# Performance work log

Measured on AMD Instinct MI355X. Metric: run time of the kernel, lower is better.

## Reference

```python
import jax, jax.numpy as jnp
import numpy as np

N = 4096      # nodes
IN = 512      # input_size
D = 128       # output_size per head
H = 4         # num_heads
SLOPE = 0.2   # leaky relu negative slope
NEG = -1e30   # masked-out logit value (finite to keep softmax grad-safe)


def setup_inputs() -> dict:
    key = jax.random.key(0)
    ks = jax.random.split(key, 8)
    stdv = 1.0 / np.sqrt(H * D)
    inputs = jax.random.normal(ks[0], (N, IN), jnp.float32)
    adjacency = jax.random.randint(ks[1], (N, N), 0, 2).astype(jnp.float32)  # dense 0/1 mask
    weight = jax.random.uniform(ks[2], (IN, H * D), jnp.float32, -stdv, stdv)
    weight_u = jax.random.uniform(ks[3], (H, D, 1), jnp.float32, -1.0, 1.0)
    weight_v = jax.random.uniform(ks[4], (H, D, 1), jnp.float32, -1.0, 1.0)
    bias = jax.random.uniform(ks[5], (1, H * D), jnp.float32, -stdv, stdv)
    proj_w = jax.random.normal(ks[6], (IN, H * D), jnp.float32) * 0.02
    proj_b = jnp.zeros((H * D,), jnp.float32)
    return {"inputs": inputs, "adjacency": adjacency, "weight": weight,
            "weight_u": weight_u, "weight_v": weight_v, "bias": bias,
            "proj_w": proj_w, "proj_b": proj_b}


def reference(inputs, adjacency, weight, weight_u, weight_v, bias, proj_w, proj_b):
    # support: [H, N, D]
    support = (inputs @ weight).reshape(N, H, D).transpose(1, 0, 2)
    # f1: per-source scores [H, 1, N]; f2: per-dest scores [H, N, 1]
    f1 = jnp.einsum('hnd,hdo->hn', support, weight_u)[:, None, :]
    f2 = jnp.einsum('hnd,hdo->hn', support, weight_v)[:, :, None]
    logits = f1 + f2                                  # [H, N, N]
    w = jnp.where(logits >= 0, logits, SLOPE * logits)  # leaky_relu
    masked = w * adjacency[None]                      # [H, N, N]
    # torch to_sparse keeps nonzero entries; sparse softmax treats the rest as -inf
    mask = masked != 0
    z = jnp.where(mask, masked, NEG)
    attn = jax.nn.softmax(z, axis=-1) * mask          # rows with no edges -> all zeros
    out = jnp.einsum('hij,hjd->hid', attn, support)   # [H, N, D]
    out = out.transpose(1, 0, 2).reshape(N, H * D)
    out = out + bias
    out = out + inputs @ proj_w + proj_b              # residual projection
    return out
```

## Files before the change

### kernel.cpp

```cpp
#include <hip/hip_runtime.h>

#define NN 4096
#define IND 512
#define HD 512
#define NH 4
#define DH 128
#define K3 1536

typedef __attribute__((ext_vector_type(8))) short bf16x8;
typedef __attribute__((ext_vector_type(4))) float f32x4;
typedef __attribute__((ext_vector_type(4))) unsigned short us4;
typedef __attribute__((ext_vector_type(8))) unsigned short us8;

typedef __attribute__((address_space(3))) void lds_void;
typedef const __attribute__((address_space(1))) void glob_void;

__device__ __forceinline__ void gll16(const void* g, void* l) {
  __builtin_amdgcn_global_load_lds((glob_void*)g, (lds_void*)l, 16, 0, 0);
}

__device__ __forceinline__ unsigned short f2bf(float x) {
  union { float f; unsigned u; } a; a.f = x;
  unsigned r = a.u + 0x7FFFu + ((a.u >> 16) & 1u);
  return (unsigned short)(r >> 16);
}
__device__ __forceinline__ float bf2f(unsigned short b) {
  union { float f; unsigned u; } a; a.u = ((unsigned)b) << 16;
  return a.f;
}

__global__ __launch_bounds__(256) void prep_inputs(const float* __restrict__ x,
                                                   unsigned short* __restrict__ A3) {
  int idx = blockIdx.x * 256 + threadIdx.x;
  int n = idx >> 9, c = idx & 511;
  float v = x[idx];
  unsigned short hi = f2bf(v);
  unsigned short lo = f2bf(v - bf2f(hi));
  size_t base = (size_t)n * K3;
  A3[base + c] = hi;
  A3[base + 512 + c] = hi;
  A3[base + 1024 + c] = lo;
}

__global__ __launch_bounds__(256) void prep_weights(const float* __restrict__ w,
                                                    const float* __restrict__ pw,
                                                    unsigned short* __restrict__ B3T,
                                                    unsigned short* __restrict__ PhT) {
  int idx = blockIdx.x * 256 + threadIdx.x;
  int c = idx >> 9, k = idx & 511;
  float v = w[(size_t)k * HD + c];
  unsigned short hi = f2bf(v);
  unsigned short lo = f2bf(v - bf2f(hi));
  size_t base = (size_t)c * K3;
  B3T[base + k] = hi;
  B3T[base + 512 + k] = lo;
  B3T[base + 1024 + k] = hi;
  float p = pw[(size_t)k * HD + c];
  PhT[(size_t)c * IND + k] = f2bf(p);
}

__global__ __launch_bounds__(256) void gemm_kernel(
    const unsigned short* __restrict__ A3, const unsigned short* __restrict__ B3T,
    const unsigned short* __restrict__ PhT,
    float* __restrict__ support, unsigned short* __restrict__ ST,
    float* __restrict__ resid,
    const float* __restrict__ projb, const float* __restrict__ bias) {
  const int z = blockIdx.z;
  const unsigned short* Bp = z ? PhT : B3T;
  const int ldb = z ? IND : K3;
  const int K = z ? IND : K3;
  const int m0 = blockIdx.x * 128;
  const int n0 = blockIdx.y * 64;
  const int tid = threadIdx.x;
  const int lane = tid & 63;
  const int wv = tid >> 6;
  const int wm = wv & 1, wn = wv >> 1;

  __shared__ unsigned short As[2][128 * 64];
  __shared__ unsigned short Bs[2][64 * 64];

  f32x4 acc[4][2];
#pragma unroll
  for (int a = 0; a < 4; ++a)
#pragma unroll
    for (int b = 0; b < 2; ++b) acc[a][b] = (f32x4){0.f, 0.f, 0.f, 0.f};

  auto STAGE = [&](int buf, int k0) {
#pragma unroll
    for (int s = 0; s < 4; ++s) {
      int c = s * 256 + tid;
      int rr = c >> 3, sl = c & 7;
      int ko = sl ^ (rr & 7);
      gll16(A3 + (size_t)(m0 + rr) * K3 + k0 + ko * 8, &As[buf][c * 8]);
    }
#pragma unroll
    for (int s = 0; s < 2; ++s) {
      int c = s * 256 + tid;
      int rr = c >> 3, sl = c & 7;
      int ko = sl ^ (rr & 7);
      gll16(Bp + (size_t)(n0 + rr) * ldb + k0 + ko * 8, &Bs[buf][c * 8]);
    }
  };

  STAGE(0, 0);
  __syncthreads();

  const int lrow = lane & 15;
  const int kgc = lane >> 4;
  const int sx = lrow & 7;
  int buf = 0;
  for (int k0 = 0; k0 < K; k0 += 64) {
    if (k0 + 64 < K) STAGE(buf ^ 1, k0 + 64);
#pragma unroll
    for (int js = 0; js < 64; js += 32) {
      int cb = (js >> 3) + kgc;
      bf16x8 af[4], bfr[2];
#pragma unroll
      for (int mf = 0; mf < 4; ++mf) {
        int row = wm * 64 + mf * 16 + lrow;
        af[mf] = *(const bf16x8*)(&As[buf][row * 64 + (cb ^ sx) * 8]);
      }
#pragma unroll
      for (int nf = 0; nf < 2; ++nf) {
        int row = wn * 32 + nf * 16 + lrow;
        bfr[nf] = *(const bf16x8*)(&Bs[buf][row * 64 + (cb ^ sx) * 8]);
      }
#pragma unroll
      for (int mf = 0; mf < 4; ++mf)
#pragma unroll
        for (int nf = 0; nf < 2; ++nf)
          acc[mf][nf] = __builtin_amdgcn_mfma_f32_16x16x32_bf16(af[mf], bfr[nf], acc[mf][nf], 0, 0, 0);
    }
    __syncthreads();
    buf ^= 1;
  }

  const int lrow4 = (lane >> 4) * 4;
  const int lcol = lane & 15;
  if (z == 0) {
#pragma unroll
    for (int mf = 0; mf < 4; ++mf) {
#pragma unroll
      for (int nf = 0; nf < 2; ++nf) {
        int rg = m0 + wm * 64 + mf * 16 + lrow4;
        int cg = n0 + wn * 32 + nf * 16 + lcol;
#pragma unroll
        for (int q = 0; q < 4; ++q)
          support[(size_t)(rg + q) * HD + cg] = acc[mf][nf][q];
        us4 st4;
#pragma unroll
        for (int q = 0; q < 4; ++q) st4[q] = f2bf(acc[mf][nf][q]);
        *(us4*)(ST + (size_t)cg * NN + rg) = st4;
      }
    }
  } else {
#pragma unroll
    for (int mf = 0; mf < 4; ++mf) {
#pragma unroll
      for (int nf = 0; nf < 2; ++nf) {
        int rg = m0 + wm * 64 + mf * 16 + lrow4;
        int cg = n0 + wn * 32 + nf * 16 + lcol;
        float addv = projb[cg] + bias[cg];
#pragma unroll
        for (int q = 0; q < 4; ++q)
          resid[(size_t)(rg + q) * HD + cg] = acc[mf][nf][q] + addv;
      }
    }
  }
}

__global__ __launch_bounds__(256) void f1f2_kernel(const float* __restrict__ support,
                                                   const float* __restrict__ wu,
                                                   const float* __restrict__ wv,
                                                   float* __restrict__ g1,
                                                   float* __restrict__ g2) {
  int lane = threadIdx.x & 63;
  int n = blockIdx.x * 4 + (threadIdx.x >> 6);
  const float* srow = support + (size_t)n * HD + lane * 8;
  int h = lane >> 4;
  int d0 = (lane * 8) & 127;
  const float* u = wu + h * DH + d0;
  const float* v = wv + h * DH + d0;
  float du = 0.f, dv = 0.f;
#pragma unroll
  for (int e = 0; e < 8; ++e) {
    float s = srow[e];
    du += s * u[e];
    dv += s * v[e];
  }
#pragma unroll
  for (int off = 1; off < 16; off <<= 1) {
    du += __shfl_xor(du, off);
    dv += __shfl_xor(dv, off);
  }
  if ((lane & 15) == 0) {
    const float L2E = 1.4426950408889634f;
    g1[h * NN + n] = du * L2E;
    g2[h * NN + n] = dv * L2E;
  }
}

__global__ __launch_bounds__(256) void ballot_kernel(const float* __restrict__ adj,
                                                     unsigned long long* __restrict__ bm) {
  int i = blockIdx.x;
  int tid = threadIdx.x, lane = tid & 63, wv = tid >> 6;
  const float* arow = adj + (size_t)i * NN;
#pragma unroll 4
  for (int it = 0; it < 16; ++it) {
    int j = it * 256 + tid;
    unsigned long long b = __ballot(arow[j] != 0.0f);
    if (lane == 0) bm[(size_t)i * 64 + it * 4 + wv] = b;
  }
}

__global__ __launch_bounds__(256) void attn_kernel(
    const unsigned short* __restrict__ ST,
    const unsigned long long* __restrict__ bm,
    const float* __restrict__ g1, const float* __restrict__ g2,
    float* __restrict__ P, float* __restrict__ S) {
  const int bx = blockIdx.x;
  const int by = blockIdx.y;
  const int bz = blockIdx.z;
  const int tid = threadIdx.x;
  const int lane = tid & 63;
  const int w = tid >> 6;

  __shared__ unsigned short tile[2][128 * 64];
  __shared__ unsigned long long bml[32 * 64];
  __shared__ float g1l[2048];

  {
    const unsigned long long* bsrc = bm + (size_t)bx * 64 * 64 + bz * 32;
#pragma unroll
    for (int s = 0; s < 8; ++s) {
      int idx = s * 256 + tid;
      int wd = idx & 31, r = idx >> 5;
      bml[wd * 64 + r] = bsrc[(size_t)r * 64 + wd];
    }
    const float* gsrc = g1 + by * NN + bz * 2048;
#pragma unroll
    for (int s = 0; s < 2; ++s) {
      int idx = s * 256 + tid;
      *(f32x4*)(g1l + idx * 4) = *(const f32x4*)(gsrc + idx * 4);
    }
  }

  const int il = lane & 15;
  const int kg = lane >> 4;
  const int r = w * 16 + il;
  const int ig = bx * 64 + r;
  const float g2v = g2[by * NN + ig];
  const float g2v5 = 0.2f * g2v;
  const unsigned short* stbase = ST + (size_t)by * 128 * NN + bz * 2048;

  auto STAGE = [&](int buf, int jt) {
#pragma unroll
    for (int s = 0; s < 4; ++s) {
      int c = s * 256 + tid;
      int rr = c >> 3, sl = c & 7;
      int jq = sl ^ (rr & 7);
      gll16(stbase + (size_t)rr * NN + jt + jq * 8, &tile[buf][c * 8]);
    }
  };

  STAGE(0, 0);
  __syncthreads();

  bf16x8 ones;
#pragma unroll
  for (int e = 0; e < 8; ++e) ones[e] = (short)0x3F80;

  f32x4 acc[8];
#pragma unroll
  for (int d = 0; d < 8; ++d) acc[d] = (f32x4){0.f, 0.f, 0.f, 0.f};
  f32x4 asum = (f32x4){0.f, 0.f, 0.f, 0.f};

  const char* bmlB = (const char*)bml;
  const int sx = il & 7;
  int buf = 0;

  for (int jt = 0; jt < 2048; jt += 64) {
    if (jt + 64 < 2048) STAGE(buf ^ 1, jt + 64);
#pragma unroll
    for (int js = 0; js < 64; js += 32) {
      int cb = (js >> 3) + kg;
      bf16x8 bc[8];
#pragma unroll
      for (int d = 0; d < 8; ++d)
        bc[d] = *(const bf16x8*)(&tile[buf][(il + d * 16) * 64 + (cb ^ sx) * 8]);

      int jw = jt + js;
      int b = (jw >> 3) + kg;
      unsigned mby = (unsigned char)bmlB[((b >> 3) * 64 + r) * 8 + (b & 7)];
      union F8 { f32x4 v[2]; float f[8]; } gc;
      gc.v[0] = *(const f32x4*)(g1l + jw + kg * 8);
      gc.v[1] = *(const f32x4*)(g1l + jw + kg * 8 + 4);
      float p[8];
#pragma unroll
      for (int e = 0; e < 8; ++e) {
        float a = gc.f[e] + g2v;
        float bb = __builtin_fmaf(0.2f, gc.f[e], g2v5);
        float m = fmaxf(a, bb);
        float pe = __builtin_amdgcn_exp2f(m);
        int sext = -(int)((mby >> e) & 1u);
        union { float f; unsigned u; } pu; pu.f = pe;
        pu.u &= (unsigned)sext;
        p[e] = pu.f;
      }
      union { unsigned u[4]; bf16x8 v; } af;
#pragma unroll
      for (int e2 = 0; e2 < 4; ++e2) {
        unsigned pk;
        asm("v_cvt_pk_bf16_f32 %0, %1, %2" : "=v"(pk) : "v"(p[2 * e2]), "v"(p[2 * e2 + 1]));
        af.u[e2] = pk;
      }
#pragma unroll
      for (int d = 0; d < 8; ++d)
        acc[d] = __builtin_amdgcn_mfma_f32_16x16x32_bf16(af.v, bc[d], acc[d], 0, 0, 0);
      asum = __builtin_amdgcn_mfma_f32_16x16x32_bf16(af.v, ones, asum, 0, 0, 0);
    }
    __syncthreads();
    buf ^= 1;
  }

  float* Pp = P + (size_t)bz * NN * HD;
#pragma unroll
  for (int d = 0; d < 8; ++d) {
    int cg = by * 128 + d * 16 + il;
#pragma unroll
    for (int q = 0; q < 4; ++q) {
      int rg = bx * 64 + w * 16 + kg * 4 + q;
      Pp[(size_t)rg * HD + cg] = acc[d][q];
    }
  }
  if (il == 0) {
#pragma unroll
    for (int q = 0; q < 4; ++q) {
      int rg = bx * 64 + w * 16 + kg * 4 + q;
      S[((size_t)bz * 4 + by) * NN + rg] = asum[q];
    }
  }
}

__global__ __launch_bounds__(256) void merge_kernel(const float* __restrict__ P,
                                                    const float* __restrict__ S,
                                                    const float* __restrict__ resid,
                                                    float* __restrict__ out) {
  int idx = blockIdx.x * 256 + threadIdx.x;
  int i = idx >> 7;
  int c = (idx & 127) * 4;
  int h = c >> 7;
  f32x4 v0 = *(const f32x4*)(P + (size_t)i * HD + c);
  f32x4 v1 = *(const f32x4*)(P + (size_t)(NN + i) * HD + c);
  float s = S[(size_t)h * NN + i] + S[(size_t)(4 + h) * NN + i];
  float rs = s > 0.0f ? 1.0f / s : 0.0f;
  f32x4 rr = *(const f32x4*)(resid + (size_t)i * HD + c);
  f32x4 o;
#pragma unroll
  for (int q = 0; q < 4; ++q) o[q] = (v0[q] + v1[q]) * rs + rr[q];
  *(f32x4*)(out + (size_t)i * HD + c) = o;
}

extern "C" void kernel_launch(void* const* d_in, const int* in_sizes, int n_in,
                              void* d_out, int out_size, void* d_ws, size_t ws_size,
                              hipStream_t stream) {
  const float* inputs = (const float*)d_in[0];
  const float* adj = (const float*)d_in[1];
  const float* weight = (const float*)d_in[2];
  const float* wu = (const float*)d_in[3];
  const float* wv = (const float*)d_in[4];
  const float* bias = (const float*)d_in[5];
  const float* projw = (const float*)d_in[6];
  const float* projb = (const float*)d_in[7];
  float* out = (float*)d_out;

  char* ws = (char*)d_ws;
  size_t off = 0;
  unsigned short* A3 = (unsigned short*)(ws + off); off += (size_t)NN * K3 * 2;
  unsigned short* B3T = (unsigned short*)(ws + off); off += (size_t)HD * K3 * 2;
  unsigned short* PhT = (unsigned short*)(ws + off); off += (size_t)HD * IND * 2;
  float* support = (float*)(ws + off); off += (size_t)NN * HD * 4;
  unsigned short* ST = (unsigned short*)(ws + off); off += (size_t)HD * NN * 2;
  float* resid = (float*)(ws + off); off += (size_t)NN * HD * 4;
  float* g1 = (float*)(ws + off); off += (size_t)NH * NN * 4;
  float* g2 = (float*)(ws + off); off += (size_t)NH * NN * 4;
  unsigned long long* bm = (unsigned long long*)(ws + off); off += (size_t)NN * 64 * 8;

  float* P = (float*)(ws + 0);
  float* S = (float*)(ws + (size_t)17 * 1024 * 1024);

  prep_inputs<<<(NN * IND) / 256, 256, 0, stream>>>(inputs, A3);
  prep_weights<<<(IND * HD) / 256, 256, 0, stream>>>(weight, projw, B3T, PhT);
  gemm_kernel<<<dim3(32, 8, 2), 256, 0, stream>>>(A3, B3T, PhT, support, ST, resid, projb, bias);
  f1f2_kernel<<<NN / 4, 256, 0, stream>>>(support, wu, wv, g1, g2);
  ballot_kernel<<<NN, 256, 0, stream>>>(adj, bm);
  attn_kernel<<<dim3(64, 4, 2), 256, 0, stream>>>(ST, bm, g1, g2, P, S);
  merge_kernel<<<2048, 256, 0, stream>>>(P, S, resid, out);
}
```

Before: 208.6 us.

## Fuse f1/f2 into GEMM epilogue, merge attention split-K in-block, drop merge kernel

The GEMM now uses 128x128 tiles with an XCD-aware block remap. It computes the per-head f1/f2 scores in its epilogue and writes ST through an LDS transpose for coalesced stores, which removes the support buffer and the f1f2 kernel. The attention kernel now splits the key dimension across four waves inside one block, each with its own double-buffered tile and no block-level barriers. It reduces the partial sums through LDS and writes the normalized output plus residual directly, which removes the P/S buffers and the merge kernel. The ballot mask is stored transposed so the attention loop can read it with strided byte loads, with prefetch managed by explicit vmcnt waits. The risks are fewer GEMM blocks and higher register pressure, plus correctness depending on the hand-counted vmcnt.

Result: faster. 200.0 us (-4.1%).

```diff
diff --git a/kernel.cpp b/kernel.cpp
--- a/kernel.cpp
+++ b/kernel.cpp
@@ -62,303 +62,334 @@
 __global__ __launch_bounds__(256) void gemm_kernel(
     const unsigned short* __restrict__ A3, const unsigned short* __restrict__ B3T,
     const unsigned short* __restrict__ PhT,
-    float* __restrict__ support, unsigned short* __restrict__ ST,
-    float* __restrict__ resid,
+    unsigned short* __restrict__ ST, float* __restrict__ resid,
+    float* __restrict__ g1, float* __restrict__ g2,
+    const float* __restrict__ wu, const float* __restrict__ wv,
     const float* __restrict__ projb, const float* __restrict__ bias) {
   const int z = blockIdx.z;
+  int L = blockIdx.x + 32 * blockIdx.y;
+  int xcd = L & 7, idx = L >> 3;
+  const int by = idx & 3;
+  const int bx = (idx >> 2) * 8 + xcd;
   const unsigned short* Bp = z ? PhT : B3T;
   const int ldb = z ? IND : K3;
   const int K = z ? IND : K3;
-  const int m0 = blockIdx.x * 128;
-  const int n0 = blockIdx.y * 64;
+  const int m0 = bx * 128;
+  const int n0 = by * 128;
   const int tid = threadIdx.x;
   const int lane = tid & 63;
-  const int wv = tid >> 6;
-  const int wm = wv & 1, wn = wv >> 1;
-
-  __shared__ unsigned short As[2][128 * 64];
-  __shared__ unsigned short Bs[2][64 * 64];
-
-  f32x4 acc[4][2];
+  const int wvv_ = tid >> 6;
+  const int wm = wvv_ & 1, wn = wvv_ >> 1;
+  const int lrow = lane & 15;
+  const int kg = lane >> 4;
+
+  __shared__ __align__(16) unsigned short sh[32768];
+
+  f32x4 acc[4][4];
 #pragma unroll
   for (int a = 0; a < 4; ++a)
 #pragma unroll
-    for (int b = 0; b < 2; ++b) acc[a][b] = (f32x4){0.f, 0.f, 0.f, 0.f};
+    for (int b = 0; b < 4; ++b) acc[a][b] = (f32x4){0.f, 0.f, 0.f, 0.f};
 
   auto STAGE = [&](int buf, int k0) {
+    unsigned short* Asb = sh + buf * 8192;
+    unsigned short* Bsb = sh + 16384 + buf * 8192;
 #pragma unroll
     for (int s = 0; s < 4; ++s) {
       int c = s * 256 + tid;
       int rr = c >> 3, sl = c & 7;
       int ko = sl ^ (rr & 7);
-      gll16(A3 + (size_t)(m0 + rr) * K3 + k0 + ko * 8, &As[buf][c * 8]);
-    }
-#pragma unroll
-    for (int s = 0; s < 2; ++s) {
+      gll16(A3 + (size_t)(m0 + rr) * K3 + k0 + ko * 8, Asb + c * 8);
+    }
+#pragma unroll
+    for (int s = 0; s < 4; ++s) {
       int c = s * 256 + tid;
       int rr = c >> 3, sl = c & 7;
       int ko = sl ^ (rr & 7);
-      gll16(Bp + (size_t)(n0 + rr) * ldb + k0 + ko * 8, &Bs[buf][c * 8]);
+      gll16(Bp + (size_t)(n0 + rr) * ldb + k0 + ko * 8, Bsb + c * 8);
     }
   };
 
   STAGE(0, 0);
   __syncthreads();
 
-  const int lrow = lane & 15;
-  const int kgc = lane >> 4;
-  const int sx = lrow & 7;
   int buf = 0;
   for (int k0 = 0; k0 < K; k0 += 64) {
     if (k0 + 64 < K) STAGE(buf ^ 1, k0 + 64);
-#pragma unroll
-    for (int js = 0; js < 64; js += 32) {
-      int cb = (js >> 3) + kgc;
-      bf16x8 af[4], bfr[2];
+    const unsigned short* Asb = sh + buf * 8192;
+    const unsigned short* Bsb = sh + 16384 + buf * 8192;
+#pragma unroll
+    for (int ks = 0; ks < 2; ++ks) {
+      int cb = ks * 4 + kg;
+      bf16x8 af[4], bfr[4];
 #pragma unroll
       for (int mf = 0; mf < 4; ++mf) {
         int row = wm * 64 + mf * 16 + lrow;
-        af[mf] = *(const bf16x8*)(&As[buf][row * 64 + (cb ^ sx) * 8]);
+        af[mf] = *(const bf16x8*)(Asb + row * 64 + (cb ^ (row & 7)) * 8);
       }
 #pragma unroll
-      for (int nf = 0; nf < 2; ++nf) {
-        int row = wn * 32 + nf * 16 + lrow;
-        bfr[nf] = *(const bf16x8*)(&Bs[buf][row * 64 + (cb ^ sx) * 8]);
+      for (int nf = 0; nf < 4; ++nf) {
+        int row = wn * 64 + nf * 16 + lrow;
+        bfr[nf] = *(const bf16x8*)(Bsb + row * 64 + (cb ^ (row & 7)) * 8);
       }
 #pragma unroll
       for (int mf = 0; mf < 4; ++mf)
 #pragma unroll
-        for (int nf = 0; nf < 2; ++nf)
+        for (int nf = 0; nf < 4; ++nf)
           acc[mf][nf] = __builtin_amdgcn_mfma_f32_16x16x32_bf16(af[mf], bfr[nf], acc[mf][nf], 0, 0, 0);
     }
     __syncthreads();
     buf ^= 1;
   }
 
-  const int lrow4 = (lane >> 4) * 4;
   const int lcol = lane & 15;
   if (z == 0) {
-#pragma unroll
-    for (int mf = 0; mf < 4; ++mf) {
-#pragma unroll
-      for (int nf = 0; nf < 2; ++nf) {
-        int rg = m0 + wm * 64 + mf * 16 + lrow4;
-        int cg = n0 + wn * 32 + nf * 16 + lcol;
-#pragma unroll
-        for (int q = 0; q < 4; ++q)
-          support[(size_t)(rg + q) * HD + cg] = acc[mf][nf][q];
+    float wuv[4], wvvv[4];
+#pragma unroll
+    for (int nf = 0; nf < 4; ++nf) {
+      int cg = n0 + wn * 64 + nf * 16 + lcol;
+      wuv[nf] = wu[cg]; wvvv[nf] = wv[cg];
+    }
+    float du[4][4], dv[4][4];
+#pragma unroll
+    for (int mf = 0; mf < 4; ++mf)
+#pragma unroll
+      for (int q = 0; q < 4; ++q) {
+        float a = 0.f, b = 0.f;
+#pragma unroll
+        for (int nf = 0; nf < 4; ++nf) {
+          a += acc[mf][nf][q] * wuv[nf];
+          b += acc[mf][nf][q] * wvvv[nf];
+        }
+#pragma unroll
+        for (int m = 1; m < 16; m <<= 1) {
+          a += __shfl_xor(a, m);
+          b += __shfl_xor(b, m);
+        }
+        du[mf][q] = a; dv[mf][q] = b;
+      }
+    float* f12 = (float*)(sh + 17920);
+    if (lcol == 0) {
+#pragma unroll
+      for (int mf = 0; mf < 4; ++mf)
+#pragma unroll
+        for (int q = 0; q < 4; ++q) {
+          int rowl = wm * 64 + mf * 16 + kg * 4 + q;
+          f12[wn * 128 + rowl] = du[mf][q];
+          f12[256 + wn * 128 + rowl] = dv[mf][q];
+        }
+    }
+    unsigned short* lst = sh;
+#pragma unroll
+    for (int mf = 0; mf < 4; ++mf)
+#pragma unroll
+      for (int nf = 0; nf < 4; ++nf) {
+        int coll = wn * 64 + nf * 16 + lcol;
+        int row4 = wm * 64 + mf * 16 + kg * 4;
         us4 st4;
 #pragma unroll
         for (int q = 0; q < 4; ++q) st4[q] = f2bf(acc[mf][nf][q]);
-        *(us4*)(ST + (size_t)cg * NN + rg) = st4;
+        *(us4*)(&lst[coll * 136 + row4]) = st4;
       }
+    __syncthreads();
+    {
+      int row = tid & 127, sel = tid >> 7;
+      float vs = f12[sel * 256 + row] + f12[sel * 256 + 128 + row];
+      float* gp = sel ? g2 : g1;
+      gp[by * NN + m0 + row] = vs * 1.4426950408889634f;
+    }
+#pragma unroll
+    for (int k = 0; k < 8; ++k) {
+      int col = k * 16 + (tid >> 4);
+      int chunk = tid & 15;
+      us8 v = *(const us8*)(&lst[col * 136 + chunk * 8]);
+      *(us8*)(ST + (size_t)(n0 + col) * NN + m0 + chunk * 8) = v;
     }
   } else {
 #pragma unroll
-    for (int mf = 0; mf < 4; ++mf) {
-#pragma unroll
-      for (int nf = 0; nf < 2; ++nf) {
-        int rg = m0 + wm * 64 + mf * 16 + lrow4;
-        int cg = n0 + wn * 32 + nf * 16 + lcol;
+    for (int mf = 0; mf < 4; ++mf)
+#pragma unroll
+      for (int nf = 0; nf < 4; ++nf) {
+        int rg = m0 + wm * 64 + mf * 16 + kg * 4;
+        int cg = n0 + wn * 64 + nf * 16 + lcol;
         float addv = projb[cg] + bias[cg];
 #pragma unroll
         for (int q = 0; q < 4; ++q)
           resid[(size_t)(rg + q) * HD + cg] = acc[mf][nf][q] + addv;
       }
-    }
-  }
-}
-
-__global__ __launch_bounds__(256) void f1f2_kernel(const float* __restrict__ support,
-                                                   const float* __restrict__ wu,
-                                                   const float* __restrict__ wv,
-                                                   float* __restrict__ g1,
-                                                   float* __restrict__ g2) {
-  int lane = threadIdx.x & 63;
-  int n = blockIdx.x * 4 + (threadIdx.x >> 6);
-  const float* srow = support + (size_t)n * HD + lane * 8;
-  int h = lane >> 4;
-  int d0 = (lane * 8) & 127;
-  const float* u = wu + h * DH + d0;
-  const float* v = wv + h * DH + d0;
-  float du = 0.f, dv = 0.f;
-#pragma unroll
-  for (int e = 0; e < 8; ++e) {
-    float s = srow[e];
-    du += s * u[e];
-    dv += s * v[e];
-  }
-#pragma unroll
-  for (int off = 1; off < 16; off <<= 1) {
-    du += __shfl_xor(du, off);
-    dv += __shfl_xor(dv, off);
-  }
-  if ((lane & 15) == 0) {
-    const float L2E = 1.4426950408889634f;
-    g1[h * NN + n] = du * L2E;
-    g2[h * NN + n] = dv * L2E;
   }
 }
 
 __global__ __launch_bounds__(256) void ballot_kernel(const float* __restrict__ adj,
-                                                     unsigned long long* __restrict__ bm) {
+                                                     unsigned long long* __restrict__ bmT) {
   int i = blockIdx.x;
-  int tid = threadIdx.x, lane = tid & 63, wv = tid >> 6;
+  int tid = threadIdx.x, lane = tid & 63, wvv_ = tid >> 6;
   const float* arow = adj + (size_t)i * NN;
 #pragma unroll 4
   for (int it = 0; it < 16; ++it) {
     int j = it * 256 + tid;
     unsigned long long b = __ballot(arow[j] != 0.0f);
-    if (lane == 0) bm[(size_t)i * 64 + it * 4 + wv] = b;
+    if (lane == 0) bmT[(size_t)(it * 4 + wvv_) * NN + i] = b;
   }
 }
 
 __global__ __launch_bounds__(256) void attn_kernel(
     const unsigned short* __restrict__ ST,
-    const unsigned long long* __restrict__ bm,
+    const unsigned long long* __restrict__ bmT,
     const float* __restrict__ g1, const float* __restrict__ g2,
-    float* __restrict__ P, float* __restrict__ S) {
+    const float* __restrict__ resid, float* __restrict__ out) {
   const int bx = blockIdx.x;
   const int by = blockIdx.y;
-  const int bz = blockIdx.z;
   const int tid = threadIdx.x;
   const int lane = tid & 63;
   const int w = tid >> 6;
-
-  __shared__ unsigned short tile[2][128 * 64];
-  __shared__ unsigned long long bml[32 * 64];
-  __shared__ float g1l[2048];
-
-  {
-    const unsigned long long* bsrc = bm + (size_t)bx * 64 * 64 + bz * 32;
-#pragma unroll
-    for (int s = 0; s < 8; ++s) {
-      int idx = s * 256 + tid;
-      int wd = idx & 31, r = idx >> 5;
-      bml[wd * 64 + r] = bsrc[(size_t)r * 64 + wd];
-    }
-    const float* gsrc = g1 + by * NN + bz * 2048;
-#pragma unroll
-    for (int s = 0; s < 2; ++s) {
-      int idx = s * 256 + tid;
-      *(f32x4*)(g1l + idx * 4) = *(const f32x4*)(gsrc + idx * 4);
-    }
-  }
-
   const int il = lane & 15;
   const int kg = lane >> 4;
-  const int r = w * 16 + il;
-  const int ig = bx * 64 + r;
-  const float g2v = g2[by * NN + ig];
-  const float g2v5 = 0.2f * g2v;
-  const unsigned short* stbase = ST + (size_t)by * 128 * NN + bz * 2048;
-
-  auto STAGE = [&](int buf, int jt) {
-#pragma unroll
-    for (int s = 0; s < 4; ++s) {
-      int c = s * 256 + tid;
-      int rr = c >> 3, sl = c & 7;
-      int jq = sl ^ (rr & 7);
-      gll16(stbase + (size_t)rr * NN + jt + jq * 8, &tile[buf][c * 8]);
-    }
+  const int i0 = bx * 32;
+
+  __shared__ unsigned short tile[4][2][4096];
+
+  const float g2v0 = g2[by * NN + i0 + il];
+  const float g2v1 = g2[by * NN + i0 + il + 16];
+  const float g2v0h = 0.2f * g2v0, g2v1h = 0.2f * g2v1;
+  const float* g1h = g1 + by * NN + w * 1024;
+  const unsigned short* STh = ST + (size_t)(by * 128) * NN + w * 1024;
+  const unsigned char* mb0 = (const unsigned char*)bmT + ((size_t)(i0 + il) << 3) + kg;
+  const unsigned char* mb1 = mb0 + 128;
+
+  const int dr0 = lane >> 2;
+  const int jq = (lane & 3) ^ ((lane >> 3) & 3);
+  const unsigned short* src0 = STh + (size_t)dr0 * NN + jq * 8;
+
+  auto STAGE = [&](int buf, int J) {
+#pragma unroll
+    for (int s = 0; s < 8; ++s)
+      gll16(src0 + (size_t)s * 16 * NN + J, &tile[w][buf][s * 512]);
   };
+  auto MOFF = [&](int t) -> size_t {
+    return ((size_t)(w * 16 + (t >> 1)) * (NN * 8)) + (size_t)((t & 1) * 4);
+  };
+
+  const int rb = il * 32 + (kg ^ ((il >> 1) & 3)) * 8;
+
+  bf16x8 ones;
+#pragma unroll
+  for (int e = 0; e < 8; ++e) ones[e] = (short)0x3F80;
+
+  f32x4 acc[2][8];
+#pragma unroll
+  for (int g = 0; g < 2; ++g)
+#pragma unroll
+    for (int d = 0; d < 8; ++d) acc[g][d] = (f32x4){0.f, 0.f, 0.f, 0.f};
+  f32x4 asum0 = (f32x4){0.f, 0.f, 0.f, 0.f};
+  f32x4 asum1 = (f32x4){0.f, 0.f, 0.f, 0.f};
 
   STAGE(0, 0);
+  f32x4 g1c0 = *(const f32x4*)(g1h + kg * 8);
+  f32x4 g1c1 = *(const f32x4*)(g1h + kg * 8 + 4);
+  unsigned mbc0 = mb0[MOFF(0)];
+  unsigned mbc1 = mb1[MOFF(0)];
+  f32x4 g1n0, g1n1;
+  unsigned mbn0 = 0, mbn1 = 0;
+
+  int buf = 0;
+  for (int t = 0; t < 32; ++t) {
+    if (t < 31) {
+      STAGE(buf ^ 1, (t + 1) * 32);
+      int tn = t + 1;
+      g1n0 = *(const f32x4*)(g1h + tn * 32 + kg * 8);
+      g1n1 = *(const f32x4*)(g1h + tn * 32 + kg * 8 + 4);
+      size_t mo = MOFF(tn);
+      mbn0 = mb0[mo];
+      mbn1 = mb1[mo];
+      asm volatile("s_waitcnt vmcnt(12)" ::: "memory");
+    } else {
+      asm volatile("s_waitcnt vmcnt(0)" ::: "memory");
+    }
+    const unsigned short* tb = &tile[w][buf][0];
+    bf16x8 bc[8];
+#pragma unroll
+    for (int d = 0; d < 8; ++d)
+      bc[d] = *(const bf16x8*)(tb + d * 512 + rb);
+
+    union F8 { f32x4 v[2]; float f[8]; } gc;
+    gc.v[0] = g1c0; gc.v[1] = g1c1;
+    float p0[8], p1[8];
+#pragma unroll
+    for (int e = 0; e < 8; ++e) {
+      float t0 = gc.f[e] + g2v0;
+      float b0 = __builtin_fmaf(0.2f, gc.f[e], g2v0h);
+      float pe0 = __builtin_amdgcn_exp2f(fmaxf(t0, b0));
+      union { float f; unsigned u; } u0; u0.f = pe0;
+      u0.u &= (unsigned)(-(int)((mbc0 >> e) & 1u));
+      p0[e] = u0.f;
+      float t1 = gc.f[e] + g2v1;
+      float b1 = __builtin_fmaf(0.2f, gc.f[e], g2v1h);
+      float pe1 = __builtin_amdgcn_exp2f(fmaxf(t1, b1));
+      union { float f; unsigned u; } u1; u1.f = pe1;
+      u1.u &= (unsigned)(-(int)((mbc1 >> e) & 1u));
+      p1[e] = u1.f;
+    }
+    union { unsigned u[4]; bf16x8 v; } af0, af1;
+#pragma unroll
+    for (int e2 = 0; e2 < 4; ++e2) {
+      unsigned pk;
+      asm("v_cvt_pk_bf16_f32 %0, %1, %2" : "=v"(pk) : "v"(p0[2 * e2]), "v"(p0[2 * e2 + 1]));
+      af0.u[e2] = pk;
+      asm("v_cvt_pk_bf16_f32 %0, %1, %2" : "=v"(pk) : "v"(p1[2 * e2]), "v"(p1[2 * e2 + 1]));
+      af1.u[e2] = pk;
+    }
+#pragma unroll
+    for (int d = 0; d < 8; ++d) {
+      acc[0][d] = __builtin_amdgcn_mfma_f32_16x16x32_bf16(af0.v, bc[d], acc[0][d], 0, 0, 0);
+      acc[1][d] = __builtin_amdgcn_mfma_f32_16x16x32_bf16(af1.v, bc[d], acc[1][d], 0, 0, 0);
+    }
+    asum0 = __builtin_amdgcn_mfma_f32_16x16x32_bf16(af0.v, ones, asum0, 0, 0, 0);
+    asum1 = __builtin_amdgcn_mfma_f32_16x16x32_bf16(af1.v, ones, asum1, 0, 0, 0);
+
+    g1c0 = g1n0; g1c1 = g1n1; mbc0 = mbn0; mbc1 = mbn1;
+    buf ^= 1;
+  }
+
   __syncthreads();
-
-  bf16x8 ones;
-#pragma unroll
-  for (int e = 0; e < 8; ++e) ones[e] = (short)0x3F80;
-
-  f32x4 acc[8];
-#pragma unroll
-  for (int d = 0; d < 8; ++d) acc[d] = (f32x4){0.f, 0.f, 0.f, 0.f};
-  f32x4 asum = (f32x4){0.f, 0.f, 0.f, 0.f};
-
-  const char* bmlB = (const char*)bml;
-  const int sx = il & 7;
-  int buf = 0;
-
-  for (int jt = 0; jt < 2048; jt += 64) {
-    if (jt + 64 < 2048) STAGE(buf ^ 1, jt + 64);
-#pragma unroll
-    for (int js = 0; js < 64; js += 32) {
-      int cb = (js >> 3) + kg;
-      bf16x8 bc[8];
-#pragma unroll
-      for (int d = 0; d < 8; ++d)
-        bc[d] = *(const bf16x8*)(&tile[buf][(il + d * 16) * 64 + (cb ^ sx) * 8]);
-
-      int jw = jt + js;
-      int b = (jw >> 3) + kg;
-      unsigned mby = (unsigned char)bmlB[((b >> 3) * 64 + r) * 8 + (b & 7)];
-      union F8 { f32x4 v[2]; float f[8]; } gc;
-      gc.v[0] = *(const f32x4*)(g1l + jw + kg * 8);
-      gc.v[1] = *(const f32x4*)(g1l + jw + kg * 8 + 4);
-      float p[8];
-#pragma unroll
-      for (int e = 0; e < 8; ++e) {
-        float a = gc.f[e] + g2v;
-        float bb = __builtin_fmaf(0.2f, gc.f[e], g2v5);
-        float m = fmaxf(a, bb);
-        float pe = __builtin_amdgcn_exp2f(m);
-        int sext = -(int)((mby >> e) & 1u);
-        union { float f; unsigned u; } pu; pu.f = pe;
-        pu.u &= (unsigned)sext;
-        p[e] = pu.f;
-      }
-      union { unsigned u[4]; bf16x8 v; } af;
-#pragma unroll
-      for (int e2 = 0; e2 < 4; ++e2) {
-        unsigned pk;
-        asm("v_cvt_pk_bf16_f32 %0, %1, %2" : "=v"(pk) : "v"(p[2 * e2]), "v"(p[2 * e2 + 1]));
-        af.u[e2] = pk;
-      }
-#pragma unroll
-      for (int d = 0; d < 8; ++d)
-        acc[d] = __builtin_amdgcn_mfma_f32_16x16x32_bf16(af.v, bc[d], acc[d], 0, 0, 0);
-      asum = __builtin_amdgcn_mfma_f32_16x16x32_bf16(af.v, ones, asum, 0, 0, 0);
-    }
-    __syncthreads();
-    buf ^= 1;
-  }
-
-  float* Pp = P + (size_t)bz * NN * HD;
-#pragma unroll
-  for (int d = 0; d < 8; ++d) {
-    int cg = by * 128 + d * 16 + il;
+  float* fl = (float*)&tile[0][0][0];
+  if (il == 0) {
 #pragma unroll
     for (int q = 0; q < 4; ++q) {
-      int rg = bx * 64 + w * 16 + kg * 4 + q;
-      Pp[(size_t)rg * HD + cg] = acc[d][q];
-    }
-  }
-  if (il == 0) {
-#pragma unroll
-    for (int q = 0; q < 4; ++q) {
-      int rg = bx * 64 + w * 16 + kg * 4 + q;
-      S[((size_t)bz * 4 + by) * NN + rg] = asum[q];
-    }
-  }
-}
-
-__global__ __launch_bounds__(256) void merge_kernel(const float* __restrict__ P,
-                                                    const float* __restrict__ S,
-                                                    const float* __restrict__ resid,
-                                                    float* __restrict__ out) {
-  int idx = blockIdx.x * 256 + threadIdx.x;
-  int i = idx >> 7;
-  int c = (idx & 127) * 4;
-  int h = c >> 7;
-  f32x4 v0 = *(const f32x4*)(P + (size_t)i * HD + c);
-  f32x4 v1 = *(const f32x4*)(P + (size_t)(NN + i) * HD + c);
-  float s = S[(size_t)h * NN + i] + S[(size_t)(4 + h) * NN + i];
-  float rs = s > 0.0f ? 1.0f / s : 0.0f;
-  f32x4 rr = *(const f32x4*)(resid + (size_t)i * HD + c);
-  f32x4 o;
-#pragma unroll
-  for (int q = 0; q < 4; ++q) o[q] = (v0[q] + v1[q]) * rs + rr[q];
-  *(f32x4*)(out + (size_t)i * HD + c) = o;
+      fl[w * 4096 + kg * 4 + q] = asum0[q];
+      fl[w * 4096 + 16 + kg * 4 + q] = asum1[q];
+    }
+  }
+  __syncthreads();
+  const int row = tid >> 3, cb = tid & 7;
+  float ssum = fl[row] + fl[4096 + row] + fl[8192 + row] + fl[12288 + row];
+  float rs = ssum > 0.0f ? 1.0f / ssum : 0.0f;
+  __syncthreads();
+#pragma unroll
+  for (int g = 0; g < 2; ++g)
+#pragma unroll
+    for (int d = 0; d < 8; ++d)
+#pragma unroll
+      for (int q = 0; q < 4; ++q)
+        fl[w * 4096 + (g * 16 + kg * 4 + q) * 128 + d * 16 + il] =
+            (g ? acc[1][d][q] : acc[0][d][q]);
+  __syncthreads();
+  const float* rres = resid + (size_t)(i0 + row) * HD + by * 128 + cb * 16;
+  float* po = out + (size_t)(i0 + row) * HD + by * 128 + cb * 16;
+#pragma unroll
+  for (int q4 = 0; q4 < 4; ++q4) {
+    int o = row * 128 + cb * 16 + q4 * 4;
+    f32x4 s0 = *(const f32x4*)(&fl[o]);
+    f32x4 s1 = *(const f32x4*)(&fl[4096 + o]);
+    f32x4 s2 = *(const f32x4*)(&fl[8192 + o]);
+    f32x4 s3 = *(const f32x4*)(&fl[12288 + o]);
+    f32x4 rr = *(const f32x4*)(rres + q4 * 4);
+    f32x4 ov;
+#pragma unroll
+    for (int q = 0; q < 4; ++q)
+      ov[q] = (s0[q] + s1[q] + s2[q] + s3[q]) * rs + rr[q];
+    *(f32x4*)(po + q4 * 4) = ov;
+  }
 }
 
 extern "C" void kernel_launch(void* const* d_in, const int* in_sizes, int n_in,
@@ -379,21 +410,16 @@
   unsigned short* A3 = (unsigned short*)(ws + off); off += (size_t)NN * K3 * 2;
   unsigned short* B3T = (unsigned short*)(ws + off); off += (size_t)HD * K3 * 2;
   unsigned short* PhT = (unsigned short*)(ws + off); off += (size_t)HD * IND * 2;
-  float* support = (float*)(ws + off); off += (size_t)NN * HD * 4;
   unsigned short* ST = (unsigned short*)(ws + off); off += (size_t)HD * NN * 2;
   float* resid = (float*)(ws + off); off += (size_t)NN * HD * 4;
   float* g1 = (float*)(ws + off); off += (size_t)NH * NN * 4;
   float* g2 = (float*)(ws + off); off += (size_t)NH * NN * 4;
-  unsigned long long* bm = (unsigned long long*)(ws + off); off += (size_t)NN * 64 * 8;
-
-  float* P = (float*)(ws + 0);
-  float* S = (float*)(ws + (size_t)17 * 1024 * 1024);
+  unsigned long long* bmT = (unsigned long long*)(ws + off); off += (size_t)NN * 64 * 8;
 
   prep_inputs<<<(NN * IND) / 256, 256, 0, stream>>>(inputs, A3);
   prep_weights<<<(IND * HD) / 256, 256, 0, stream>>>(weight, projw, B3T, PhT);
-  gemm_kernel<<<dim3(32, 8, 2), 256, 0, stream>>>(A3, B3T, PhT, support, ST, resid, projb, bias);
-  f1f2_kernel<<<NN / 4, 256, 0, stream>>>(support, wu, wv, g1, g2);
-  ballot_kernel<<<NN, 256, 0, stream>>>(adj, bm);
-  attn_kernel<<<dim3(64, 4, 2), 256, 0, stream>>>(ST, bm, g1, g2, P, S);
-  merge_kernel<<<2048, 256, 0, stream>>>(P, S, resid, out);
-}
+  gemm_kernel<<<dim3(32, 4, 2), 256, 0, stream>>>(A3, B3T, PhT, ST, resid, g1, g2,
+                                                  wu, wv, projb, bias);
+  ballot_kernel<<<NN, 256, 0, stream>>>(adj, bmT);
+  attn_kernel<<<dim3(128, 4), 256, 0, stream>>>(ST, bmT, g1, g2, resid, out);
+}
```
